# Performance work log

Hardware: AMD Instinct MI355X
Metric: run time of the kernel (lower is better)

Reference implementation:

```python
import jax, jax.numpy as jnp
import numpy as np

N_ITEMS = 100000
N_USERS = 16384
HIST = 50
TEXT_DIM = 256
GCN_DIM = 128
HIDDEN_DIM = 512
TOWER_DIM = 128


def _l2norm(x, eps=1e-12):
    # F.normalize(dim=1): x / max(||x||, eps)
    n = jnp.sqrt(jnp.sum(x * x, axis=1, keepdims=True))
    return x / jnp.maximum(n, eps)


def setup_inputs() -> dict:
    key = jax.random.key(0)
    ks = jax.random.split(key, 10)
    s1i = 1.0 / np.sqrt(TEXT_DIM + GCN_DIM)
    s2i = 1.0 / np.sqrt(HIDDEN_DIM)
    s1u = 1.0 / np.sqrt(GCN_DIM + TOWER_DIM)
    return {
        "item_text_emb": jax.random.normal(ks[0], (N_ITEMS, TEXT_DIM), jnp.float32),
        "gcn_item_emb": jax.random.normal(ks[1], (N_ITEMS, GCN_DIM), jnp.float32),
        "gcn_user_emb": jax.random.normal(ks[2], (N_USERS, GCN_DIM), jnp.float32),
        "hist_idx": jax.random.randint(ks[3], (N_USERS, HIST), 0, N_ITEMS),
        "W1i": jax.random.normal(ks[4], (TEXT_DIM + GCN_DIM, HIDDEN_DIM), jnp.float32) * s1i,
        "b1i": jnp.zeros((HIDDEN_DIM,), jnp.float32),
        "W2i": jax.random.normal(ks[5], (HIDDEN_DIM, TOWER_DIM), jnp.float32) * s2i,
        "b2i": jnp.zeros((TOWER_DIM,), jnp.float32),
        "W1u": jax.random.normal(ks[6], (GCN_DIM + TOWER_DIM, HIDDEN_DIM), jnp.float32) * s1u,
        "b1u": jnp.zeros((HIDDEN_DIM,), jnp.float32),
        "W2u": jax.random.normal(ks[7], (HIDDEN_DIM, TOWER_DIM), jnp.float32) * s2i,
        "b2u": jnp.zeros((TOWER_DIM,), jnp.float32),
    }


def reference(item_text_emb, gcn_item_emb, gcn_user_emb, hist_idx,
              W1i, b1i, W2i, b2i, W1u, b1u, W2u, b2u):
    # encode_items: MLP over concat(text, gcn) features, then L2 normalize
    item_feat = jnp.concatenate([item_text_emb, gcn_item_emb], axis=1)  # [N_items, text+gcn]
    h = jax.nn.relu(item_feat @ W1i + b1i)
    item_emb = _l2norm(h @ W2i + b2i)  # [N_items, TOWER_DIM]
    # encode_users: per-user gather of history item embeddings + mean pooling
    hist = jnp.mean(item_emb[hist_idx], axis=1)  # [N_users, TOWER_DIM]
    fused = jnp.concatenate([gcn_user_emb, hist], axis=1)
    hu = jax.nn.relu(fused @ W1u + b1u)
    user_emb = _l2norm(hu @ W2u + b2u)  # [N_users, TOWER_DIM]
    return user_emb
```

## Files before the change

kernel.cpp:

```cpp
#include <hip/hip_runtime.h>
#include <hip/hip_bf16.h>

#define HIST 50

typedef __bf16 bf8 __attribute__((ext_vector_type(8)));
typedef float  f4  __attribute__((ext_vector_type(4)));

__device__ __forceinline__ unsigned short f2bf(float x) {
    unsigned u = __builtin_bit_cast(unsigned, x);
    u += 0x7fffu + ((u >> 16) & 1u);
    return (unsigned short)(u >> 16);
}
__device__ __forceinline__ float bf2f(unsigned b) {
    unsigned u = b << 16;
    return __builtin_bit_cast(float, u);
}

__global__ void pack_weights(const float* __restrict__ W1i, const float* __restrict__ W2i,
                             const float* __restrict__ W1u, const float* __restrict__ W2u,
                             unsigned short* __restrict__ dstbase)
{
    int i = blockIdx.x * 256 + threadIdx.x;
    const float* W; unsigned short* dst; int N, KS, loc;
    if (i < 24576)      { W = W1i; dst = dstbase;          N = 512; KS = 12; loc = i; }
    else if (i < 32768) { W = W2i; dst = dstbase + 196608; N = 128; KS = 16; loc = i - 24576; }
    else if (i < 49152) { W = W1u; dst = dstbase + 262144; N = 512; KS = 8;  loc = i - 32768; }
    else                { W = W2u; dst = dstbase + 393216; N = 128; KS = 16; loc = i - 49152; }
    int l = loc & 63, fi = loc >> 6;
    int ks = fi % KS, nt = fi / KS;
    int q = l >> 4, c = l & 15;
    const float* src = W + (size_t)(ks * 32 + q * 8) * N + nt * 16 + c;
    unsigned o[4];
    #pragma unroll
    for (int k = 0; k < 4; ++k) {
        unsigned lo = f2bf(src[(2 * k) * N]);
        unsigned hi = f2bf(src[(2 * k + 1) * N]);
        o[k] = lo | (hi << 16);
    }
    uint4 v; v.x = o[0]; v.y = o[1]; v.z = o[2]; v.w = o[3];
    ((uint4*)dst)[(size_t)(nt * KS + ks) * 64 + l] = v;
}

template<int KS1, int ASTR, bool OUT_BF16>
__device__ __forceinline__ void two_layer(
    unsigned short* U,
    const float* b1s, const float* b2s, float* sumsq,
    const bf8* __restrict__ w1f, const bf8* __restrict__ w2f,
    void* __restrict__ outp, int row0, int tid)
{
    const int HSTR = 520;
    const int l = tid & 63, w = tid >> 6;
    const int q = l >> 4, c = l & 15;

    f4 acc1[2][8];
    #pragma unroll
    for (int i = 0; i < 2; ++i)
        #pragma unroll
        for (int j = 0; j < 8; ++j) acc1[i][j] = (f4)0.0f;

    const unsigned short* a0p = U + c * ASTR + q * 8;
    const unsigned short* a1p = U + (16 + c) * ASTR + q * 8;
    const bf8* wp = w1f + (size_t)(w * 8) * KS1 * 64 + l;
    #pragma unroll
    for (int ks = 0; ks < KS1; ++ks) {
        bf8 a0 = *(const bf8*)(a0p + ks * 32);
        bf8 a1 = *(const bf8*)(a1p + ks * 32);
        #pragma unroll
        for (int nt = 0; nt < 8; ++nt) {
            bf8 b = wp[(size_t)nt * KS1 * 64 + ks * 64];
            acc1[0][nt] = __builtin_amdgcn_mfma_f32_16x16x32_bf16(a0, b, acc1[0][nt], 0, 0, 0);
            acc1[1][nt] = __builtin_amdgcn_mfma_f32_16x16x32_bf16(a1, b, acc1[1][nt], 0, 0, 0);
        }
    }
    __syncthreads();
    unsigned short* Hs = U;
    #pragma unroll
    for (int nt = 0; nt < 8; ++nt) {
        int col = (w * 8 + nt) * 16 + c;
        float bias = b1s[col];
        #pragma unroll
        for (int rt = 0; rt < 2; ++rt)
            #pragma unroll
            for (int reg = 0; reg < 4; ++reg) {
                float h = fmaxf(acc1[rt][nt][reg] + bias, 0.0f);
                Hs[(rt * 16 + q * 4 + reg) * HSTR + col] = f2bf(h);
            }
    }
    __syncthreads();

    f4 acc2[2][2];
    #pragma unroll
    for (int i = 0; i < 2; ++i)
        #pragma unroll
        for (int j = 0; j < 2; ++j) acc2[i][j] = (f4)0.0f;

    const unsigned short* h0p = Hs + c * HSTR + q * 8;
    const unsigned short* h1p = Hs + (16 + c) * HSTR + q * 8;
    #pragma unroll
    for (int ks = 0; ks < 16; ++ks) {
        bf8 a0 = *(const bf8*)(h0p + ks * 32);
        bf8 a1 = *(const bf8*)(h1p + ks * 32);
        #pragma unroll
        for (int j = 0; j < 2; ++j) {
            bf8 b = w2f[(size_t)((w * 2 + j) * 16 + ks) * 64 + l];
            acc2[0][j] = __builtin_amdgcn_mfma_f32_16x16x32_bf16(a0, b, acc2[0][j], 0, 0, 0);
            acc2[1][j] = __builtin_amdgcn_mfma_f32_16x16x32_bf16(a1, b, acc2[1][j], 0, 0, 0);
        }
    }
    float v[2][2][4];
    #pragma unroll
    for (int rt = 0; rt < 2; ++rt)
        #pragma unroll
        for (int j = 0; j < 2; ++j)
            #pragma unroll
            for (int reg = 0; reg < 4; ++reg)
                v[rt][j][reg] = acc2[rt][j][reg] + b2s[(w * 2 + j) * 16 + c];
    #pragma unroll
    for (int rt = 0; rt < 2; ++rt)
        #pragma unroll
        for (int reg = 0; reg < 4; ++reg) {
            float s = v[rt][0][reg] * v[rt][0][reg] + v[rt][1][reg] * v[rt][1][reg];
            s += __shfl_xor(s, 1); s += __shfl_xor(s, 2);
            s += __shfl_xor(s, 4); s += __shfl_xor(s, 8);
            if (c == 0) atomicAdd(&sumsq[rt * 16 + q * 4 + reg], s);
        }
    __syncthreads();
    #pragma unroll
    for (int rt = 0; rt < 2; ++rt)
        #pragma unroll
        for (int reg = 0; reg < 4; ++reg) {
            int row = rt * 16 + q * 4 + reg;
            float inv = 1.0f / fmaxf(sqrtf(sumsq[row]), 1e-12f);
            #pragma unroll
            for (int j = 0; j < 2; ++j) {
                int col = (w * 2 + j) * 16 + c;
                float o = v[rt][j][reg] * inv;
                if (OUT_BF16)
                    ((unsigned short*)outp)[(size_t)(row0 + row) * 128 + col] = f2bf(o);
                else
                    ((float*)outp)[(size_t)(row0 + row) * 128 + col] = o;
            }
        }
}

__global__ __launch_bounds__(256, 4) void item_kernel(
    const float* __restrict__ text, const float* __restrict__ gcn,
    const bf8* __restrict__ w1f, const float* __restrict__ b1,
    const bf8* __restrict__ w2f, const float* __restrict__ b2,
    unsigned short* __restrict__ item_bf)
{
    __shared__ __align__(16) unsigned short U[32 * 520];
    __shared__ float b1s[512], b2s[128], sumsq[32];
    const int tid = threadIdx.x;
    const int row0 = blockIdx.x * 32;
    const float4* t4 = (const float4*)text;
    const float4* g4 = (const float4*)gcn;
    #pragma unroll
    for (int j = 0; j < 8; ++j) {
        int idx = tid + j * 256; int r = idx >> 6, c4 = idx & 63;
        float4 x = t4[(size_t)(row0 + r) * 64 + c4];
        ushort4 s; s.x = f2bf(x.x); s.y = f2bf(x.y); s.z = f2bf(x.z); s.w = f2bf(x.w);
        *(ushort4*)(U + r * 392 + c4 * 4) = s;
    }
    #pragma unroll
    for (int j = 0; j < 4; ++j) {
        int idx = tid + j * 256; int r = idx >> 5, c4 = idx & 31;
        float4 x = g4[(size_t)(row0 + r) * 32 + c4];
        ushort4 s; s.x = f2bf(x.x); s.y = f2bf(x.y); s.z = f2bf(x.z); s.w = f2bf(x.w);
        *(ushort4*)(U + r * 392 + 256 + c4 * 4) = s;
    }
    b1s[tid] = b1[tid]; b1s[tid + 256] = b1[tid + 256];
    if (tid < 128) b2s[tid] = b2[tid];
    if (tid < 32)  sumsq[tid] = 0.0f;
    __syncthreads();
    two_layer<12, 392, true>(U, b1s, b2s, sumsq, w1f, w2f, item_bf, row0, tid);
}

__global__ __launch_bounds__(256, 4) void user_kernel(
    const float* __restrict__ gcnu, const int* __restrict__ hist,
    const unsigned short* __restrict__ item_bf,
    const bf8* __restrict__ w1f, const float* __restrict__ b1,
    const bf8* __restrict__ w2f, const float* __restrict__ b2,
    float* __restrict__ outp)
{
    __shared__ __align__(16) unsigned short U[32 * 520];
    __shared__ float b1s[512], b2s[128], sumsq[32];
    const int tid = threadIdx.x;
    const int u0 = blockIdx.x * 32;
    int* histL = (int*)(U + 32 * 272);
    const float4* g4 = (const float4*)gcnu;
    #pragma unroll
    for (int j = 0; j < 4; ++j) {
        int idx = tid + j * 256; int r = idx >> 5, c4 = idx & 31;
        float4 x = g4[(size_t)(u0 + r) * 32 + c4];
        ushort4 s; s.x = f2bf(x.x); s.y = f2bf(x.y); s.z = f2bf(x.z); s.w = f2bf(x.w);
        *(ushort4*)(U + r * 272 + c4 * 4) = s;
    }
    for (int i = tid; i < 32 * HIST; i += 256)
        histL[i] = hist[(size_t)u0 * HIST + i];
    b1s[tid] = b1[tid]; b1s[tid + 256] = b1[tid + 256];
    if (tid < 128) b2s[tid] = b2[tid];
    if (tid < 32)  sumsq[tid] = 0.0f;
    __syncthreads();
    {
        const int u = tid >> 3, g = tid & 7;
        float f[16];
        #pragma unroll
        for (int k = 0; k < 16; ++k) f[k] = 0.0f;
        const int* hrow = histL + u * HIST;
        #pragma unroll 5
        for (int t = 0; t < HIST; ++t) {
            int id = hrow[t];
            const uint4* p = (const uint4*)(item_bf + (size_t)id * 128 + g * 16);
            uint4 x0 = p[0], x1 = p[1];
            unsigned vs[8] = {x0.x, x0.y, x0.z, x0.w, x1.x, x1.y, x1.z, x1.w};
            #pragma unroll
            for (int k = 0; k < 8; ++k) {
                f[2 * k]     += bf2f(vs[k] & 0xffffu);
                f[2 * k + 1] += bf2f(vs[k] >> 16);
            }
        }
        unsigned o[8];
        #pragma unroll
        for (int k = 0; k < 8; ++k)
            o[k] = (unsigned)f2bf(f[2 * k] * 0.02f) | ((unsigned)f2bf(f[2 * k + 1] * 0.02f) << 16);
        uint4 s0; s0.x = o[0]; s0.y = o[1]; s0.z = o[2]; s0.w = o[3];
        uint4 s1; s1.x = o[4]; s1.y = o[5]; s1.z = o[6]; s1.w = o[7];
        *(uint4*)(U + u * 272 + 128 + g * 16) = s0;
        *(uint4*)(U + u * 272 + 128 + g * 16 + 8) = s1;
    }
    __syncthreads();
    two_layer<8, 272, false>(U, b1s, b2s, sumsq, w1f, w2f, outp, u0, tid);
}

extern "C" void kernel_launch(void* const* d_in, const int* in_sizes, int n_in,
                              void* d_out, int out_size, void* d_ws, size_t ws_size,
                              hipStream_t stream) {
    const float* text = (const float*)d_in[0];
    const float* gcni = (const float*)d_in[1];
    const float* gcnu = (const float*)d_in[2];
    const int*   hist = (const int*)d_in[3];
    const float* W1i  = (const float*)d_in[4];
    const float* b1i  = (const float*)d_in[5];
    const float* W2i  = (const float*)d_in[6];
    const float* b2i  = (const float*)d_in[7];
    const float* W1u  = (const float*)d_in[8];
    const float* b1u  = (const float*)d_in[9];
    const float* W2u  = (const float*)d_in[10];
    const float* b2u  = (const float*)d_in[11];
    float* out = (float*)d_out;

    unsigned short* itemb = (unsigned short*)d_ws;
    unsigned short* pw = itemb + 12800000;

    pack_weights<<<224, 256, 0, stream>>>(W1i, W2i, W1u, W2u, pw);
    item_kernel<<<100000 / 32, 256, 0, stream>>>(
        text, gcni, (const bf8*)pw, b1i, (const bf8*)(pw + 196608), b2i, itemb);
    user_kernel<<<16384 / 32, 256, 0, stream>>>(
        gcnu, hist, itemb, (const bf8*)(pw + 262144), b1u, (const bf8*)(pw + 393216), b2u, out);
}
```

Baseline: 366.9 us.

## Retile item MLP kernel to 128-row blocks with chunked hidden-layer fusion

The item encoder now processes 128 rows per block instead of 32. Each wave computes a 64x64 output tile, and the 512-wide hidden layer is handled in four 128-column chunks that feed straight into the second GEMM's accumulators. Weight fragments are reused across four row tiles instead of two, which cuts global weight traffic per item. The cost is about 140KB of LDS per block, so occupancy drops to one block per CU, along with more register pressure and extra barriers per chunk.

```diff
diff --git a/kernel.cpp b/kernel.cpp
--- a/kernel.cpp
+++ b/kernel.cpp
@@ -2,6 +2,7 @@
 #include <hip/hip_bf16.h>
 
 #define HIST 50
+#define N_ITEMS 100000
 
 typedef __bf16 bf8 __attribute__((ext_vector_type(8)));
 typedef float  f4  __attribute__((ext_vector_type(4)));
@@ -41,6 +42,149 @@
     ((uint4*)dst)[(size_t)(nt * KS + ks) * 64 + l] = v;
 }
 
+#define RS 392
+#define HSd 136
+
+__global__ __launch_bounds__(256, 1) void item_kernel(
+    const float* __restrict__ text, const float* __restrict__ gcn,
+    const bf8* __restrict__ w1f, const float* __restrict__ b1,
+    const bf8* __restrict__ w2f, const float* __restrict__ b2,
+    unsigned short* __restrict__ item_bf)
+{
+    __shared__ __align__(16) unsigned short As[128 * RS];
+    __shared__ __align__(16) unsigned short Hs[128 * HSd];
+    __shared__ float b1s[512], b2s[128], sumsq[128];
+    const int tid = threadIdx.x;
+    const int row0 = blockIdx.x * 128;
+    const int nval = min(128, N_ITEMS - row0);
+
+    const float4* t4 = (const float4*)text;
+    const float4* g4 = (const float4*)gcn;
+    #pragma unroll
+    for (int j = 0; j < 32; ++j) {
+        int idx = tid + j * 256; int r = idx >> 6, c4 = idx & 63;
+        float4 x = (r < nval) ? t4[(size_t)(row0 + r) * 64 + c4] : make_float4(0.f,0.f,0.f,0.f);
+        ushort4 s; s.x = f2bf(x.x); s.y = f2bf(x.y); s.z = f2bf(x.z); s.w = f2bf(x.w);
+        *(ushort4*)(As + r * RS + c4 * 4) = s;
+    }
+    #pragma unroll
+    for (int j = 0; j < 16; ++j) {
+        int idx = tid + j * 256; int r = idx >> 5, c4 = idx & 31;
+        float4 x = (r < nval) ? g4[(size_t)(row0 + r) * 32 + c4] : make_float4(0.f,0.f,0.f,0.f);
+        ushort4 s; s.x = f2bf(x.x); s.y = f2bf(x.y); s.z = f2bf(x.z); s.w = f2bf(x.w);
+        *(ushort4*)(As + r * RS + 256 + c4 * 4) = s;
+    }
+    b1s[tid] = b1[tid]; b1s[tid + 256] = b1[tid + 256];
+    if (tid < 128) { b2s[tid] = b2[tid]; sumsq[tid] = 0.0f; }
+    __syncthreads();
+
+    const int l = tid & 63, w = tid >> 6;
+    const int q = l >> 4, c = l & 15;
+    const int rbase = (w & 1) * 64;
+    const int cbase = (w >> 1) * 64;
+
+    f4 acc2[4][4];
+    #pragma unroll
+    for (int i = 0; i < 4; ++i)
+        #pragma unroll
+        for (int j = 0; j < 4; ++j) acc2[i][j] = (f4)0.0f;
+
+    const unsigned short* ap = As + (size_t)(rbase + c) * RS + q * 8;
+    const unsigned short* hp = Hs + (size_t)(rbase + c) * HSd + q * 8;
+
+    #pragma unroll 1
+    for (int cc = 0; cc < 4; ++cc) {
+        f4 acc1[4][4];
+        #pragma unroll
+        for (int i = 0; i < 4; ++i)
+            #pragma unroll
+            for (int j = 0; j < 4; ++j) acc1[i][j] = (f4)0.0f;
+
+        const bf8* w1p = w1f + (size_t)((cc * 8 + (w >> 1) * 4) * 12) * 64 + l;
+        #pragma unroll
+        for (int ks = 0; ks < 12; ++ks) {
+            bf8 a[4], b[4];
+            #pragma unroll
+            for (int rt = 0; rt < 4; ++rt)
+                a[rt] = *(const bf8*)(ap + rt * 16 * RS + ks * 32);
+            #pragma unroll
+            for (int nt = 0; nt < 4; ++nt)
+                b[nt] = w1p[(size_t)(nt * 12 + ks) * 64];
+            #pragma unroll
+            for (int rt = 0; rt < 4; ++rt)
+                #pragma unroll
+                for (int nt = 0; nt < 4; ++nt)
+                    acc1[rt][nt] = __builtin_amdgcn_mfma_f32_16x16x32_bf16(a[rt], b[nt], acc1[rt][nt], 0, 0, 0);
+        }
+
+        if (cc > 0) __syncthreads();
+        #pragma unroll
+        for (int nt = 0; nt < 4; ++nt) {
+            float bias = b1s[cc * 128 + cbase + nt * 16 + c];
+            #pragma unroll
+            for (int rt = 0; rt < 4; ++rt)
+                #pragma unroll
+                for (int reg = 0; reg < 4; ++reg) {
+                    float h = fmaxf(acc1[rt][nt][reg] + bias, 0.0f);
+                    Hs[(size_t)(rbase + rt * 16 + q * 4 + reg) * HSd + cbase + nt * 16 + c] = f2bf(h);
+                }
+        }
+        __syncthreads();
+
+        #pragma unroll
+        for (int ks2 = 0; ks2 < 4; ++ks2) {
+            bf8 a[4], b[4];
+            #pragma unroll
+            for (int rt = 0; rt < 4; ++rt)
+                a[rt] = *(const bf8*)(hp + rt * 16 * HSd + ks2 * 32);
+            #pragma unroll
+            for (int nt = 0; nt < 4; ++nt)
+                b[nt] = w2f[(size_t)(((cbase >> 4) + nt) * 16 + cc * 4 + ks2) * 64 + l];
+            #pragma unroll
+            for (int rt = 0; rt < 4; ++rt)
+                #pragma unroll
+                for (int nt = 0; nt < 4; ++nt)
+                    acc2[rt][nt] = __builtin_amdgcn_mfma_f32_16x16x32_bf16(a[rt], b[nt], acc2[rt][nt], 0, 0, 0);
+        }
+    }
+
+    float v[4][4][4];
+    #pragma unroll
+    for (int rt = 0; rt < 4; ++rt)
+        #pragma unroll
+        for (int nt = 0; nt < 4; ++nt) {
+            float bias = b2s[cbase + nt * 16 + c];
+            #pragma unroll
+            for (int reg = 0; reg < 4; ++reg)
+                v[rt][nt][reg] = acc2[rt][nt][reg] + bias;
+        }
+    #pragma unroll
+    for (int rt = 0; rt < 4; ++rt)
+        #pragma unroll
+        for (int reg = 0; reg < 4; ++reg) {
+            float s = 0.f;
+            #pragma unroll
+            for (int nt = 0; nt < 4; ++nt) s += v[rt][nt][reg] * v[rt][nt][reg];
+            s += __shfl_xor(s, 1); s += __shfl_xor(s, 2);
+            s += __shfl_xor(s, 4); s += __shfl_xor(s, 8);
+            if (c == 0) atomicAdd(&sumsq[rbase + rt * 16 + q * 4 + reg], s);
+        }
+    __syncthreads();
+    #pragma unroll
+    for (int rt = 0; rt < 4; ++rt)
+        #pragma unroll
+        for (int reg = 0; reg < 4; ++reg) {
+            int row = rbase + rt * 16 + q * 4 + reg;
+            if (row < nval) {
+                float inv = 1.0f / fmaxf(sqrtf(sumsq[row]), 1e-12f);
+                #pragma unroll
+                for (int nt = 0; nt < 4; ++nt)
+                    item_bf[(size_t)(row0 + row) * 128 + cbase + nt * 16 + c] =
+                        f2bf(v[rt][nt][reg] * inv);
+            }
+        }
+}
+
 template<int KS1, int ASTR, bool OUT_BF16>
 __device__ __forceinline__ void two_layer(
     unsigned short* U,
@@ -73,7 +217,7 @@
         }
     }
     __syncthreads();
-    unsigned short* Hs = U;
+    unsigned short* Hsu = U;
     #pragma unroll
     for (int nt = 0; nt < 8; ++nt) {
         int col = (w * 8 + nt) * 16 + c;
@@ -83,7 +227,7 @@
             #pragma unroll
             for (int reg = 0; reg < 4; ++reg) {
                 float h = fmaxf(acc1[rt][nt][reg] + bias, 0.0f);
-                Hs[(rt * 16 + q * 4 + reg) * HSTR + col] = f2bf(h);
+                Hsu[(rt * 16 + q * 4 + reg) * HSTR + col] = f2bf(h);
             }
     }
     __syncthreads();
@@ -94,8 +238,8 @@
         #pragma unroll
         for (int j = 0; j < 2; ++j) acc2[i][j] = (f4)0.0f;
 
-    const unsigned short* h0p = Hs + c * HSTR + q * 8;
-    const unsigned short* h1p = Hs + (16 + c) * HSTR + q * 8;
+    const unsigned short* h0p = Hsu + c * HSTR + q * 8;
+    const unsigned short* h1p = Hsu + (16 + c) * HSTR + q * 8;
     #pragma unroll
     for (int ks = 0; ks < 16; ++ks) {
         bf8 a0 = *(const bf8*)(h0p + ks * 32);
@@ -141,39 +285,6 @@
                     ((float*)outp)[(size_t)(row0 + row) * 128 + col] = o;
             }
         }
-}
-
-__global__ __launch_bounds__(256, 4) void item_kernel(
-    const float* __restrict__ text, const float* __restrict__ gcn,
-    const bf8* __restrict__ w1f, const float* __restrict__ b1,
-    const bf8* __restrict__ w2f, const float* __restrict__ b2,
-    unsigned short* __restrict__ item_bf)
-{
-    __shared__ __align__(16) unsigned short U[32 * 520];
-    __shared__ float b1s[512], b2s[128], sumsq[32];
-    const int tid = threadIdx.x;
-    const int row0 = blockIdx.x * 32;
-    const float4* t4 = (const float4*)text;
-    const float4* g4 = (const float4*)gcn;
-    #pragma unroll
-    for (int j = 0; j < 8; ++j) {
-        int idx = tid + j * 256; int r = idx >> 6, c4 = idx & 63;
-        float4 x = t4[(size_t)(row0 + r) * 64 + c4];
-        ushort4 s; s.x = f2bf(x.x); s.y = f2bf(x.y); s.z = f2bf(x.z); s.w = f2bf(x.w);
-        *(ushort4*)(U + r * 392 + c4 * 4) = s;
-    }
-    #pragma unroll
-    for (int j = 0; j < 4; ++j) {
-        int idx = tid + j * 256; int r = idx >> 5, c4 = idx & 31;
-        float4 x = g4[(size_t)(row0 + r) * 32 + c4];
-        ushort4 s; s.x = f2bf(x.x); s.y = f2bf(x.y); s.z = f2bf(x.z); s.w = f2bf(x.w);
-        *(ushort4*)(U + r * 392 + 256 + c4 * 4) = s;
-    }
-    b1s[tid] = b1[tid]; b1s[tid + 256] = b1[tid + 256];
-    if (tid < 128) b2s[tid] = b2[tid];
-    if (tid < 32)  sumsq[tid] = 0.0f;
-    __syncthreads();
-    two_layer<12, 392, true>(U, b1s, b2s, sumsq, w1f, w2f, item_bf, row0, tid);
 }
 
 __global__ __launch_bounds__(256, 4) void user_kernel(
@@ -254,7 +365,7 @@
     unsigned short* pw = itemb + 12800000;
 
     pack_weights<<<224, 256, 0, stream>>>(W1i, W2i, W1u, W2u, pw);
-    item_kernel<<<100000 / 32, 256, 0, stream>>>(
+    item_kernel<<<(N_ITEMS + 127) / 128, 256, 0, stream>>>(
         text, gcni, (const bf8*)pw, b1i, (const bf8*)(pw + 196608), b2i, itemb);
     user_kernel<<<16384 / 32, 256, 0, stream>>>(
         gcnu, hist, itemb, (const bf8*)(pw + 262144), b1u, (const bf8*)(pw + 393216), b2u, out);
```

Result: slower. 452.1 us (+23.2%).
